# Optimization experiments

Hardware: AMD Instinct MI355X
Metric: run time of the kernel (lower is better)

## Reference

```python
import jax, jax.numpy as jnp
import numpy as np

B, C, H, W = 4, 128, 128, 128
HEADS, DHEAD = 8, C // 8
N = H * W
NEG_SLOPE = 0.2
LN_EPS = 1e-5


def _build_grid_edges(h, w):
    # 3x3 neighborhood including self (matches the torch double loop),
    # then append N extra self loops (add_self_loops in the module).
    rows, cols = [], []
    for r in range(h):
        for c in range(w):
            idx = r * w + c
            for dr in (-1, 0, 1):
                for dc in (-1, 0, 1):
                    nr, nc = r + dr, c + dc
                    if 0 <= nr < h and 0 <= nc < w:
                        rows.append(idx)
                        cols.append(nr * w + nc)
    rows += list(range(h * w))
    cols += list(range(h * w))
    return np.asarray(rows, np.int32), np.asarray(cols, np.int32)

_SRC_NP, _DST_NP = _build_grid_edges(H, W)  # PyG: messages flow src -> dst
SRC = jnp.asarray(_SRC_NP)
DST = jnp.asarray(_DST_NP)


def setup_inputs() -> dict:
    key = jax.random.key(0)
    ks = jax.random.split(key, 7)
    s_lin = 1.0 / np.sqrt(C)
    return {
        "x": jax.random.normal(ks[0], (B, C, H, W), jnp.float32),
        "W_lin": jax.random.normal(ks[1], (C, HEADS * DHEAD), jnp.float32) * s_lin,
        "att_src": jax.random.normal(ks[2], (HEADS, DHEAD), jnp.float32) * s_lin,
        "att_dst": jax.random.normal(ks[3], (HEADS, DHEAD), jnp.float32) * s_lin,
        "bias": jnp.zeros((C,), jnp.float32),
        "gamma": jnp.ones((C,), jnp.float32),
        "beta": jnp.zeros((C,), jnp.float32),
    }


def _gat_forward(x, W_lin, att_src, att_dst, bias, gamma, beta):
    b = x.shape[0]
    x_nodes = x.reshape(b, C, N).transpose(0, 2, 1)            # [B,N,C]
    xp = (x_nodes @ W_lin).reshape(b, N, HEADS, DHEAD)          # [B,N,H,D]
    a_src = jnp.einsum('bnhd,hd->bnh', xp, att_src)             # [B,N,H]
    a_dst = jnp.einsum('bnhd,hd->bnh', xp, att_dst)
    score = jax.nn.leaky_relu(a_src[:, SRC] + a_dst[:, DST], NEG_SLOPE)  # [B,E,H]

    def seg_softmax(s):  # [E,H] softmax over edges grouped by DST
        m = jax.ops.segment_max(s, DST, num_segments=N)
        e = jnp.exp(s - m[DST])
        den = jax.ops.segment_sum(e, DST, num_segments=N)
        return e / den[DST]

    alpha = jax.vmap(seg_softmax)(score)                        # [B,E,H]
    msg = xp[:, SRC] * alpha[..., None]                         # [B,E,H,D]
    agg = jax.vmap(lambda m: jax.ops.segment_sum(m, DST, num_segments=N))(msg)
    out = agg.reshape(b, N, C) + bias                           # GATConv bias
    out = jax.nn.elu(out)
    # LayerNorm over channel dim
    mu = out.mean(-1, keepdims=True)
    var = out.var(-1, keepdims=True)
    out = (out - mu) * jax.lax.rsqrt(var + LN_EPS) * gamma + beta
    return out.transpose(0, 2, 1).reshape(b, C, H, W)


def reference(x, W_lin, att_src, att_dst, bias, gamma, beta):
    return _gat_forward(x, W_lin, att_src, att_dst, bias, gamma, beta)
```

## Files before the change

### kernel.cpp

```cpp
#include <hip/hip_runtime.h>
#include <stdint.h>

#define BATCH  4
#define CCH    128
#define GRID_H 128
#define GRID_W 128
#define NNODE  (GRID_H*GRID_W)
#define NHEAD  8
#define DH     16
#define XPW    144
#define WPAD   68

typedef __attribute__((ext_vector_type(8))) short short8;
typedef __attribute__((ext_vector_type(4))) float f32x4;
typedef __attribute__((ext_vector_type(4))) unsigned u32x4;

__device__ inline unsigned short f2bf(float f){
    unsigned u = __float_as_uint(f);
    return (unsigned short)((u + 0x7FFFu + ((u >> 16) & 1u)) >> 16);
}
__device__ inline unsigned packbf(float a, float b){
    return (unsigned)f2bf(a) | ((unsigned)f2bf(b) << 16);
}

__global__ void kW(const float* __restrict__ Wl, const float* __restrict__ attS,
                   const float* __restrict__ attD, unsigned* __restrict__ Wb)
{
    __shared__ float Wa[8][16];
    const int t = threadIdx.x;
    const int cbase = blockIdx.x * 8;
    if (t < 128){
        int cl = t >> 4, j = t & 15;
        const float* av = (j < 8 ? attS + j*DH : attD + (j-8)*DH);
        const float* wr = Wl + (size_t)(cbase + cl)*CCH + (j & 7)*DH;
        float s = 0.f;
        #pragma unroll
        for (int d = 0; d < DH; ++d) s += wr[d]*av[d];
        Wa[cl][j] = s;
    }
    __syncthreads();
    for (int it = 0; it < 3; ++it){
        int flat = it*256 + t;
        if (flat < 576){
            int k2l = flat / 144, co = flat % 144;
            int k2 = blockIdx.x*4 + k2l;
            float w0, w1;
            if (co < CCH){
                w0 = Wl[(size_t)(2*k2)*CCH + co];
                w1 = Wl[(size_t)(2*k2+1)*CCH + co];
            } else {
                w0 = Wa[2*k2l][co-CCH];
                w1 = Wa[2*k2l+1][co-CCH];
            }
            Wb[co*WPAD + k2] = packbf(w0, w1);
        }
    }
}

__global__ __launch_bounds__(256, 2) void kA(
    const float* __restrict__ x, const unsigned* __restrict__ Wbg,
    float* __restrict__ xp2)
{
    __shared__ __align__(16) unsigned WbL[XPW*WPAD];
    __shared__ __align__(16) unsigned Xa[64*WPAD];

    const int t  = threadIdx.x;
    const int b  = blockIdx.y;
    const int n0 = blockIdx.x * 64;

    #pragma unroll
    for (int it = 0; it < 10; ++it){
        int flat4 = it*256 + t;
        if (flat4 < (XPW*WPAD)/4){
            u32x4 v = *(const u32x4*)(Wbg + flat4*4);
            *(u32x4*)(&WbL[flat4*4]) = v;
        }
    }
    const float* xb = x + (size_t)b*CCH*NNODE + n0;
    {
        const int g = t & 15;
        #pragma unroll
        for (int it = 0; it < 4; ++it){
            int c2 = (t >> 4) + it*16;
            const float* p0 = xb + (size_t)(2*c2)*NNODE + 4*g;
            f32x4 v0 = *(const f32x4*)p0;
            f32x4 v1 = *(const f32x4*)(p0 + NNODE);
            #pragma unroll
            for (int i = 0; i < 4; ++i)
                Xa[(4*g+i)*WPAD + c2] = packbf(v0[i], v1[i]);
        }
    }
    __syncthreads();

    const int w = t >> 6, lane = t & 63;
    const int col = lane & 15, q = lane >> 4;
    const int row = w*16 + col;

    f32x4 acc[9];
    #pragma unroll
    for (int ct = 0; ct < 9; ++ct) acc[ct] = (f32x4)(0.f);

    union U { u32x4 u; short8 s; };
    #pragma unroll
    for (int kc = 0; kc < 4; ++kc){
        const int kof = kc*16 + q*4;
        U fa; fa.u = *(const u32x4*)(&Xa[row*WPAD + kof]);
        #pragma unroll
        for (int ct = 0; ct < 9; ++ct){
            U fb; fb.u = *(const u32x4*)(&WbL[(ct*16+col)*WPAD + kof]);
            acc[ct] = __builtin_amdgcn_mfma_f32_16x16x32_bf16(fa.s, fb.s, acc[ct], 0, 0, 0);
        }
    }

    float* xr = xp2 + (size_t)b*NNODE*XPW;
    #pragma unroll
    for (int ct = 0; ct < 9; ++ct){
        #pragma unroll
        for (int r = 0; r < 4; ++r){
            const int n = n0 + w*16 + q*4 + r;
            xr[(size_t)n*XPW + ct*16 + col] = acc[ct][r];
        }
    }
}

__global__ __launch_bounds__(256, 4) void kB(
    const float* __restrict__ xp2, const float* __restrict__ bias,
    const float* __restrict__ gamma, const float* __restrict__ beta,
    float* __restrict__ out)
{
    __shared__ float outT[CCH][33];
    const int t = threadIdx.x, w = t >> 6, l = t & 63;
    const int b  = blockIdx.y;
    const int n0 = blockIdx.x * 32;
    const float* xpb = xp2 + (size_t)b*NNODE*XPW;
    const int h = l >> 3;
    const float2 bi = *(const float2*)(bias  + 2*l);
    const float2 ga = *(const float2*)(gamma + 2*l);
    const float2 be = *(const float2*)(beta  + 2*l);

    for (int i = 0; i < 8; ++i){
        const int nl = w*8 + i;
        const int n  = n0 + nl;
        const int rr = n >> 7, cc = n & 127;

        int srcv[9]; bool val[9];
        #pragma unroll
        for (int e = 0; e < 9; ++e){
            const int dr = e/3 - 1, dc = e%3 - 1;
            const bool v = ((unsigned)(rr+dr) < GRID_H) && ((unsigned)(cc+dc) < GRID_W);
            val[e]  = v;
            srcv[e] = v ? (n + dr*GRID_W + dc) : n;
        }
        const float ad = xpb[(size_t)n*XPW + 136 + h];
        float asv[9];
        #pragma unroll
        for (int e = 0; e < 9; ++e) asv[e] = xpb[(size_t)srcv[e]*XPW + 128 + h];
        float2 xv[9];
        #pragma unroll
        for (int e = 0; e < 9; ++e) xv[e] = *(const float2*)(xpb + (size_t)srcv[e]*XPW + 2*l);

        float s[9], m = -1e30f;
        #pragma unroll
        for (int e = 0; e < 9; ++e){
            float sc = asv[e] + ad;
            sc = sc > 0.f ? sc : 0.2f*sc;
            s[e] = val[e] ? sc : -1e30f;
            m = fmaxf(m, s[e]);
        }
        float wt[9], den = 0.f;
        #pragma unroll
        for (int e = 0; e < 9; ++e){
            float ex = __expf(s[e] - m);
            wt[e] = val[e] ? ex : 0.f;
            den += wt[e];
        }
        den += wt[4];
        const float inv = 1.f / den;

        float a0 = 0.f, a1 = 0.f;
        #pragma unroll
        for (int e = 0; e < 9; ++e){
            float f = wt[e] * inv;
            if (e == 4) f *= 2.f;
            a0 += f * xv[e].x;
            a1 += f * xv[e].y;
        }

        float o0 = a0 + bi.x, o1 = a1 + bi.y;
        o0 = o0 > 0.f ? o0 : __expf(o0) - 1.f;
        o1 = o1 > 0.f ? o1 : __expf(o1) - 1.f;

        float sm = o0 + o1, sq = o0*o0 + o1*o1;
        #pragma unroll
        for (int off = 32; off >= 1; off >>= 1){
            sm += __shfl_xor(sm, off, 64);
            sq += __shfl_xor(sq, off, 64);
        }
        const float mu  = sm * (1.f/128.f);
        float var = sq * (1.f/128.f) - mu*mu;
        var = var < 0.f ? 0.f : var;
        const float rstd = rsqrtf(var + 1e-5f);
        outT[2*l  ][nl] = (o0 - mu)*rstd*ga.x + be.x;
        outT[2*l+1][nl] = (o1 - mu)*rstd*ga.y + be.y;
    }
    __syncthreads();

    float* ob = out + (size_t)b*CCH*NNODE + n0;
    #pragma unroll
    for (int it = 0; it < 16; ++it){
        int c = it*8 + (t >> 5);
        int coln = t & 31;
        ob[(size_t)c*NNODE + coln] = outT[c][coln];
    }
}

extern "C" void kernel_launch(void* const* d_in, const int* in_sizes, int n_in,
                              void* d_out, int out_size, void* d_ws, size_t ws_size,
                              hipStream_t stream)
{
    const float* x    = (const float*)d_in[0];
    const float* Wl   = (const float*)d_in[1];
    const float* attS = (const float*)d_in[2];
    const float* attD = (const float*)d_in[3];
    const float* bias = (const float*)d_in[4];
    const float* gamma= (const float*)d_in[5];
    const float* beta = (const float*)d_in[6];
    float* out = (float*)d_out;

    float*    xp2 = (float*)d_ws;
    unsigned* Wb  = (unsigned*)(xp2 + (size_t)BATCH*NNODE*XPW);

    kW<<<dim3(16), 256, 0, stream>>>(Wl, attS, attD, Wb);
    kA<<<dim3(NNODE/64, BATCH), 256, 0, stream>>>(x, Wb, xp2);
    kB<<<dim3(NNODE/32, BATCH), 256, 0, stream>>>(xp2, bias, gamma, beta, out);
}
```

Measured before the change: 134.4 us.

## Store projected features as bf16 with separate score buffer; process two nodes per wave

The projection kernel now writes the 128 feature channels as bf16 and the 16 attention scores as fp32 into a separate interleaved buffer. This replaces the 144-wide fp32 intermediate and roughly halves the intermediate traffic between the two kernels. The projection kernel now does 128 nodes per block with two MFMA row tiles per wave, and the aggregation kernel handles two nodes per wave with 4 channels per lane, using fast rcp/rsq intrinsics. The cost is lower precision in the aggregated features and more register pressure.

Result: faster. 122.4 us (-8.9%).

```diff
diff --git a/kernel.cpp b/kernel.cpp
--- a/kernel.cpp
+++ b/kernel.cpp
@@ -8,8 +8,8 @@
 #define NNODE  (GRID_H*GRID_W)
 #define NHEAD  8
 #define DH     16
-#define XPW    144
 #define WPAD   68
+#define WROWS  144
 
 typedef __attribute__((ext_vector_type(8))) short short8;
 typedef __attribute__((ext_vector_type(4))) float f32x4;
@@ -22,6 +22,8 @@
 __device__ inline unsigned packbf(float a, float b){
     return (unsigned)f2bf(a) | ((unsigned)f2bf(b) << 16);
 }
+__device__ inline float bflo(unsigned u){ return __uint_as_float(u << 16); }
+__device__ inline float bfhi(unsigned u){ return __uint_as_float(u & 0xFFFF0000u); }
 
 __global__ void kW(const float* __restrict__ Wl, const float* __restrict__ attS,
                    const float* __restrict__ attD, unsigned* __restrict__ Wb)
@@ -59,29 +61,27 @@
 
 __global__ __launch_bounds__(256, 2) void kA(
     const float* __restrict__ x, const unsigned* __restrict__ Wbg,
-    float* __restrict__ xp2)
-{
-    __shared__ __align__(16) unsigned WbL[XPW*WPAD];
-    __shared__ __align__(16) unsigned Xa[64*WPAD];
+    unsigned short* __restrict__ xpb, float* __restrict__ scb)
+{
+    __shared__ __align__(16) unsigned WbL[WROWS*WPAD];
+    __shared__ __align__(16) unsigned Xa[128*WPAD];
 
     const int t  = threadIdx.x;
     const int b  = blockIdx.y;
-    const int n0 = blockIdx.x * 64;
+    const int n0 = blockIdx.x * 128;
 
     #pragma unroll
     for (int it = 0; it < 10; ++it){
-        int flat4 = it*256 + t;
-        if (flat4 < (XPW*WPAD)/4){
-            u32x4 v = *(const u32x4*)(Wbg + flat4*4);
-            *(u32x4*)(&WbL[flat4*4]) = v;
-        }
+        int f4 = it*256 + t;
+        if (f4 < (WROWS*WPAD)/4)
+            *(u32x4*)(&WbL[f4*4]) = *(const u32x4*)(Wbg + (size_t)f4*4);
     }
     const float* xb = x + (size_t)b*CCH*NNODE + n0;
     {
-        const int g = t & 15;
-        #pragma unroll
-        for (int it = 0; it < 4; ++it){
-            int c2 = (t >> 4) + it*16;
+        const int g = t & 31, c2b = t >> 5;
+        #pragma unroll
+        for (int it = 0; it < 8; ++it){
+            int c2 = c2b + it*8;
             const float* p0 = xb + (size_t)(2*c2)*NNODE + 4*g;
             f32x4 v0 = *(const f32x4*)p0;
             f32x4 v1 = *(const f32x4*)(p0 + NNODE);
@@ -94,123 +94,142 @@
 
     const int w = t >> 6, lane = t & 63;
     const int col = lane & 15, q = lane >> 4;
-    const int row = w*16 + col;
-
-    f32x4 acc[9];
-    #pragma unroll
-    for (int ct = 0; ct < 9; ++ct) acc[ct] = (f32x4)(0.f);
+
+    f32x4 acc[2][9];
+    #pragma unroll
+    for (int mi = 0; mi < 2; ++mi)
+        #pragma unroll
+        for (int ct = 0; ct < 9; ++ct) acc[mi][ct] = (f32x4)(0.f);
 
     union U { u32x4 u; short8 s; };
     #pragma unroll
     for (int kc = 0; kc < 4; ++kc){
         const int kof = kc*16 + q*4;
-        U fa; fa.u = *(const u32x4*)(&Xa[row*WPAD + kof]);
+        U fa0, fa1;
+        fa0.u = *(const u32x4*)(&Xa[((2*w+0)*16+col)*WPAD + kof]);
+        fa1.u = *(const u32x4*)(&Xa[((2*w+1)*16+col)*WPAD + kof]);
         #pragma unroll
         for (int ct = 0; ct < 9; ++ct){
             U fb; fb.u = *(const u32x4*)(&WbL[(ct*16+col)*WPAD + kof]);
-            acc[ct] = __builtin_amdgcn_mfma_f32_16x16x32_bf16(fa.s, fb.s, acc[ct], 0, 0, 0);
-        }
-    }
-
-    float* xr = xp2 + (size_t)b*NNODE*XPW;
-    #pragma unroll
-    for (int ct = 0; ct < 9; ++ct){
+            acc[0][ct] = __builtin_amdgcn_mfma_f32_16x16x32_bf16(fa0.s, fb.s, acc[0][ct], 0, 0, 0);
+            acc[1][ct] = __builtin_amdgcn_mfma_f32_16x16x32_bf16(fa1.s, fb.s, acc[1][ct], 0, 0, 0);
+        }
+    }
+
+    unsigned short* xr = xpb + (size_t)b*NNODE*CCH;
+    float*          sr = scb + (size_t)b*NNODE*16;
+    const int sidx = (col < 8) ? 2*col : 2*(col-8)+1;
+    #pragma unroll
+    for (int mi = 0; mi < 2; ++mi){
         #pragma unroll
         for (int r = 0; r < 4; ++r){
-            const int n = n0 + w*16 + q*4 + r;
-            xr[(size_t)n*XPW + ct*16 + col] = acc[ct][r];
+            const int n = n0 + (2*w+mi)*16 + q*4 + r;
+            #pragma unroll
+            for (int ct = 0; ct < 8; ++ct)
+                xr[(size_t)n*CCH + ct*16 + col] = f2bf(acc[mi][ct][r]);
+            sr[(size_t)n*16 + sidx] = acc[mi][8][r];
         }
     }
 }
 
 __global__ __launch_bounds__(256, 4) void kB(
-    const float* __restrict__ xp2, const float* __restrict__ bias,
-    const float* __restrict__ gamma, const float* __restrict__ beta,
-    float* __restrict__ out)
-{
-    __shared__ float outT[CCH][33];
-    const int t = threadIdx.x, w = t >> 6, l = t & 63;
+    const unsigned short* __restrict__ xpb, const float* __restrict__ scb,
+    const float* __restrict__ bias, const float* __restrict__ gamma,
+    const float* __restrict__ beta, float* __restrict__ out)
+{
+    __shared__ float outT[CCH][65];
+    const int t = threadIdx.x, w = t >> 6, lane = t & 63;
+    const int h2 = lane >> 5, l2 = lane & 31;
     const int b  = blockIdx.y;
-    const int n0 = blockIdx.x * 32;
-    const float* xpb = xp2 + (size_t)b*NNODE*XPW;
-    const int h = l >> 3;
-    const float2 bi = *(const float2*)(bias  + 2*l);
-    const float2 ga = *(const float2*)(gamma + 2*l);
-    const float2 be = *(const float2*)(beta  + 2*l);
+    const int n0 = blockIdx.x * 64;
+    const uint2*  xvb = (const uint2*)(xpb + (size_t)b*NNODE*CCH);
+    const float2* scB = (const float2*)(scb + (size_t)b*NNODE*16);
+    const int h = l2 >> 2;
+    const f32x4 bi = *(const f32x4*)(bias  + 4*l2);
+    const f32x4 ga = *(const f32x4*)(gamma + 4*l2);
+    const f32x4 be = *(const f32x4*)(beta  + 4*l2);
 
     for (int i = 0; i < 8; ++i){
-        const int nl = w*8 + i;
+        const int nl = w*16 + 2*i + h2;
         const int n  = n0 + nl;
         const int rr = n >> 7, cc = n & 127;
-
-        int srcv[9]; bool val[9];
+        const bool vU = rr > 0, vD = rr < GRID_H-1, vL = cc > 0, vR = cc < GRID_W-1;
+
+        bool val[9]; int src[9];
         #pragma unroll
         for (int e = 0; e < 9; ++e){
             const int dr = e/3 - 1, dc = e%3 - 1;
-            const bool v = ((unsigned)(rr+dr) < GRID_H) && ((unsigned)(cc+dc) < GRID_W);
-            val[e]  = v;
-            srcv[e] = v ? (n + dr*GRID_W + dc) : n;
-        }
-        const float ad = xpb[(size_t)n*XPW + 136 + h];
-        float asv[9];
-        #pragma unroll
-        for (int e = 0; e < 9; ++e) asv[e] = xpb[(size_t)srcv[e]*XPW + 128 + h];
-        float2 xv[9];
-        #pragma unroll
-        for (int e = 0; e < 9; ++e) xv[e] = *(const float2*)(xpb + (size_t)srcv[e]*XPW + 2*l);
-
+            const bool vr_ = (dr < 0) ? vU : (dr > 0 ? vD : true);
+            const bool vc_ = (dc < 0) ? vL : (dc > 0 ? vR : true);
+            val[e] = vr_ && vc_;
+            src[e] = val[e] ? (n + dr*GRID_W + dc) : n;
+        }
+        float2 sc[9];
+        #pragma unroll
+        for (int e = 0; e < 9; ++e) sc[e] = scB[src[e]*8 + h];
+        uint2 xv[9];
+        #pragma unroll
+        for (int e = 0; e < 9; ++e) xv[e] = xvb[(size_t)src[e]*32 + l2];
+
+        const float ad = sc[4].y;
         float s[9], m = -1e30f;
         #pragma unroll
         for (int e = 0; e < 9; ++e){
-            float sc = asv[e] + ad;
-            sc = sc > 0.f ? sc : 0.2f*sc;
-            s[e] = val[e] ? sc : -1e30f;
+            float sv = sc[e].x + ad;
+            sv = fmaxf(sv, 0.2f*sv);
+            s[e] = val[e] ? sv : -1e30f;
             m = fmaxf(m, s[e]);
         }
         float wt[9], den = 0.f;
         #pragma unroll
         for (int e = 0; e < 9; ++e){
             float ex = __expf(s[e] - m);
-            wt[e] = val[e] ? ex : 0.f;
-            den += wt[e];
+            ex = val[e] ? ex : 0.f;
+            wt[e] = ex; den += ex;
         }
         den += wt[4];
-        const float inv = 1.f / den;
-
-        float a0 = 0.f, a1 = 0.f;
+        const float inv = __builtin_amdgcn_rcpf(den);
+
+        float a0 = 0.f, a1 = 0.f, a2 = 0.f, a3 = 0.f;
         #pragma unroll
         for (int e = 0; e < 9; ++e){
             float f = wt[e] * inv;
-            if (e == 4) f *= 2.f;
-            a0 += f * xv[e].x;
-            a1 += f * xv[e].y;
-        }
-
-        float o0 = a0 + bi.x, o1 = a1 + bi.y;
+            if (e == 4) f += f;
+            a0 += f * bflo(xv[e].x);
+            a1 += f * bfhi(xv[e].x);
+            a2 += f * bflo(xv[e].y);
+            a3 += f * bfhi(xv[e].y);
+        }
+
+        float o0 = a0 + bi[0], o1 = a1 + bi[1], o2 = a2 + bi[2], o3 = a3 + bi[3];
         o0 = o0 > 0.f ? o0 : __expf(o0) - 1.f;
         o1 = o1 > 0.f ? o1 : __expf(o1) - 1.f;
-
-        float sm = o0 + o1, sq = o0*o0 + o1*o1;
-        #pragma unroll
-        for (int off = 32; off >= 1; off >>= 1){
+        o2 = o2 > 0.f ? o2 : __expf(o2) - 1.f;
+        o3 = o3 > 0.f ? o3 : __expf(o3) - 1.f;
+
+        float sm = (o0 + o1) + (o2 + o3);
+        float sq = o0*o0 + o1*o1 + o2*o2 + o3*o3;
+        #pragma unroll
+        for (int off = 1; off <= 16; off <<= 1){
             sm += __shfl_xor(sm, off, 64);
             sq += __shfl_xor(sq, off, 64);
         }
         const float mu  = sm * (1.f/128.f);
         float var = sq * (1.f/128.f) - mu*mu;
         var = var < 0.f ? 0.f : var;
-        const float rstd = rsqrtf(var + 1e-5f);
-        outT[2*l  ][nl] = (o0 - mu)*rstd*ga.x + be.x;
-        outT[2*l+1][nl] = (o1 - mu)*rstd*ga.y + be.y;
+        const float rstd = __builtin_amdgcn_rsqf(var + 1e-5f);
+        outT[4*l2+0][nl] = (o0 - mu)*rstd*ga[0] + be[0];
+        outT[4*l2+1][nl] = (o1 - mu)*rstd*ga[1] + be[1];
+        outT[4*l2+2][nl] = (o2 - mu)*rstd*ga[2] + be[2];
+        outT[4*l2+3][nl] = (o3 - mu)*rstd*ga[3] + be[3];
     }
     __syncthreads();
 
     float* ob = out + (size_t)b*CCH*NNODE + n0;
     #pragma unroll
-    for (int it = 0; it < 16; ++it){
-        int c = it*8 + (t >> 5);
-        int coln = t & 31;
-        ob[(size_t)c*NNODE + coln] = outT[c][coln];
+    for (int it = 0; it < 32; ++it){
+        int c = it*4 + w;
+        ob[(size_t)c*NNODE + lane] = outT[c][lane];
     }
 }
 
@@ -227,10 +246,11 @@
     const float* beta = (const float*)d_in[6];
     float* out = (float*)d_out;
 
-    float*    xp2 = (float*)d_ws;
-    unsigned* Wb  = (unsigned*)(xp2 + (size_t)BATCH*NNODE*XPW);
+    unsigned short* xpb = (unsigned short*)d_ws;
+    float*          scb = (float*)(xpb + (size_t)BATCH*NNODE*CCH);
+    unsigned*       Wb  = (unsigned*)(scb + (size_t)BATCH*NNODE*16);
 
     kW<<<dim3(16), 256, 0, stream>>>(Wl, attS, attD, Wb);
-    kA<<<dim3(NNODE/64, BATCH), 256, 0, stream>>>(x, Wb, xp2);
-    kB<<<dim3(NNODE/32, BATCH), 256, 0, stream>>>(xp2, bias, gamma, beta, out);
-}
+    kA<<<dim3(NNODE/128, BATCH), 256, 0, stream>>>(x, Wb, xpb, scb);
+    kB<<<dim3(NNODE/64, BATCH), 256, 0, stream>>>(xpb, scb, bias, gamma, beta, out);
+}
```
